# Performance work log

Measured on AMD Instinct MI355X. Metric: run time of the kernel, lower is better.

## Reference

```python
import jax, jax.numpy as jnp
import numpy as np

T, B, V = 512, 64, 1296
S = 30            # fixed target length per sample (targets are concatenated B*S)
BLANK = 0
NEG = -1e30       # -inf surrogate, safe under logaddexp


def setup_inputs() -> dict:
    key = jax.random.key(0)
    k1, k2, k3 = jax.random.split(key, 3)
    logits = jax.random.normal(k1, (T, B, V), dtype=jnp.float32)
    log_probs = jax.nn.log_softmax(logits, axis=-1)  # valid log-prob input to CTC
    # targets are gloss ids in [1, V) (blank=0 excluded), concatenated layout
    targets = jax.random.randint(k2, (B * S,), 1, V, dtype=jnp.int64)
    input_lengths = jax.random.randint(k3, (B,), T // 2, T + 1, dtype=jnp.int32)
    target_lengths = jnp.full((B,), S, dtype=jnp.int32)
    return {"log_probs": log_probs, "targets": targets,
            "input_lengths": input_lengths, "target_lengths": target_lengths}


def _ctc_loss(log_probs, targets2d, input_lengths, target_lengths):
    # log_probs: (T,B,V); targets2d: (B,S)
    L = 2 * S + 1
    b_idx = jnp.arange(B)
    # extended label sequence with interleaved blanks: (B, L)
    ext = jnp.zeros((B, L), dtype=targets2d.dtype).at[:, 1::2].set(targets2d)
    # emission log-probs on lattice positions: lp[t,b,l] = log_probs[t,b,ext[b,l]]
    lp = jnp.take_along_axis(log_probs,
                             jnp.broadcast_to(ext[None, :, :], (T, B, L)), axis=2)
    # skip transition allowed where ext[l] != blank and ext[l] != ext[l-2]
    ext_m2 = jnp.pad(ext[:, :-2], ((0, 0), (2, 0)), constant_values=BLANK)
    allow = (ext != BLANK) & (ext != ext_m2)  # (B, L)

    alpha0 = jnp.full((B, L), NEG, dtype=log_probs.dtype)
    alpha0 = alpha0.at[:, 0].set(lp[0, :, 0]).at[:, 1].set(lp[0, :, 1])

    def step(alpha, lp_t):
        prev1 = jnp.pad(alpha[:, :-1], ((0, 0), (1, 0)), constant_values=NEG)
        prev2 = jnp.pad(alpha[:, :-2], ((0, 0), (2, 0)), constant_values=NEG)
        m = jnp.logaddexp(alpha, prev1)
        m = jnp.where(allow, jnp.logaddexp(m, prev2), m)
        new = m + lp_t
        return new, new

    _, alphas = jax.lax.scan(step, alpha0, lp[1:])          # (T-1, B, L)
    alphas = jnp.concatenate([alpha0[None], alphas], axis=0)  # (T, B, L)

    # alpha at each sample's final frame
    alpha_T = alphas[input_lengths - 1, b_idx]               # (B, L)
    tl = target_lengths.astype(jnp.int32)
    a_last_blank = alpha_T[b_idx, 2 * tl]
    a_last_label = alpha_T[b_idx, 2 * tl - 1]
    loss = -jnp.logaddexp(a_last_blank, a_last_label)        # (B,)
    # zero_infinity=True: infeasible alignments contribute 0
    loss = jnp.where(loss >= 1e29, 0.0, loss)
    # reduction='mean': per-sample loss / target_length, then batch mean
    return jnp.mean(loss / target_lengths.astype(loss.dtype))


def reference(log_probs, targets, input_lengths, target_lengths):
    targets2d = targets.reshape(B, S)  # all target_lengths == S (concatenated layout)
    return _ctc_loss(log_probs, targets2d, input_lengths, target_lengths)
```

## Files before the change

kernel.cpp:

```cpp
#include <hip/hip_runtime.h>

#define T_DIM 512
#define B_DIM 64
#define V_DIM 1296
#define S_DIM 30
#define LN2   0.6931471805599453f

typedef float v2f __attribute__((ext_vector_type(2)));

template<int CTRL, bool BC>
__device__ __forceinline__ float dppf(float src, float old) {
    return __int_as_float(__builtin_amdgcn_update_dpp(
        __float_as_int(old), __float_as_int(src), CTRL, 0xF, 0xF, BC));
}

template<int MODE>
__device__ __forceinline__ void consume_chunk(const float4* __restrict__ ringc,
                                              int c, int len, int lane, v2f S,
                                              v2f& X, v2f& Y, int& E)
{
    const int jl = lane & 15;
    float4 buf[8];
#pragma unroll
    for (int i = 0; i < 8; ++i) buf[i] = ringc[i * 16 + jl];

    float mred = 0.f;
#pragma unroll
    for (int i = 0; i < 32; ++i) {
        float4 w = buf[i & 7];
        if (i + 8 < 32) buf[i & 7] = ringc[(i + 8) * 16 + jl];

        if (MODE == 0 && i == 0) {
            bool l0 = (lane == 0);
            X = (v2f){ l0 ? ldexpf(w.z, 64) : 0.f, 0.f };
            Y = (v2f){ l0 ? ldexpf(w.x, 64) : 0.f, 0.f };
            E = 64;
        } else {
            float q3m = dppf<0x111, true>(Y.y, 0.f);
            v2f Z  = { q3m, Y.x };
            v2f T1 = X + Z;
            v2f T2 = X + Y;
            v2f T3 = __builtin_elementwise_fma(S, Z, T2);
            v2f Wb = { w.z, w.w };
            v2f Wl = { w.x, w.y };
            v2f Xn = T1 * Wb;
            v2f Yn = T3 * Wl;
            if (MODE == 2) {
                bool act = (c * 32 + i) < len;
                X = act ? Xn : X;
                Y = act ? Yn : Y;
            } else { X = Xn; Y = Yn; }
        }

        if ((i & 7) == 3) mred = fmaxf(fmaxf(X.x, X.y), fmaxf(Y.x, Y.y));
        if ((i & 7) == 4) mred = fmaxf(mred, dppf<0x111, true>(mred, 0.f));
        if ((i & 7) == 5) mred = fmaxf(mred, dppf<0x112, true>(mred, 0.f));
        if ((i & 7) == 6) mred = fmaxf(mred, dppf<0x114, true>(mred, 0.f));
        if ((i & 7) == 7) {
            mred = fmaxf(mred, dppf<0x118, true>(mred, 0.f));
            int e15 = (__builtin_amdgcn_readlane(__float_as_int(mred), 15) >> 23) & 0xFF;
            int s = 191 - e15;
            X = (v2f){ ldexpf(X.x, s), ldexpf(X.y, s) };
            Y = (v2f){ ldexpf(Y.x, s), ldexpf(Y.y, s) };
            E += s;
        }
    }
}

struct PReg { float a, b, c; };

__device__ __forceinline__ PReg load_rows(const float* __restrict__ lpb,
                                          int k, int r, int lab0, int lab1)
{
    const float* row = lpb + (size_t)(k * 32 + r) * (B_DIM * V_DIM);
    PReg x;
    x.a = row[lab0];
    x.b = row[lab1];
    x.c = row[0];
    return x;
}

__device__ __forceinline__ void write_chunk(float4* __restrict__ ring, int k, int p,
                                            int q, const PReg& x)
{
    float wz = __expf(x.c);
    float wx = (q < 15) ? __expf(x.a) : 0.f;
    float wy = (q < 15) ? __expf(x.b) : 0.f;
    ring[(size_t)(k & 3) * 512 + p] = make_float4(wx, wy, wz, wz);
}

__global__ __launch_bounds__(576)
void ctc_fused_kernel(const float* __restrict__ log_probs,
                      const int*   __restrict__ targets,
                      const int*   __restrict__ input_lengths,
                      const int*   __restrict__ target_lengths,
                      float*       __restrict__ losses,
                      unsigned*    __restrict__ counter,
                      float*       __restrict__ out)
{
    __shared__ float4 ring[4 * 512];
    const int  b    = blockIdx.x;
    const int  tid  = threadIdx.x;
    const int  len  = input_lengths[b];
    const bool prod = (tid < 512);

    const int q = tid & 15;
    const int r = (tid & 511) >> 4;
    int lab0 = 0, lab1 = 0;
    PReg rA = {0,0,0}, rB = {0,0,0};
    const float* lpb = log_probs + (size_t)b * V_DIM;

    const int lane = tid - 512;
    v2f X = {0.f, 0.f}, Y = {0.f, 0.f}, S = {0.f, 0.f};
    int E = 0;

    if (prod) {
        int i0 = b * S_DIM + ((2 * q     < S_DIM) ? 2 * q     : 0);
        int i1 = b * S_DIM + ((2 * q + 1 < S_DIM) ? 2 * q + 1 : 0);
        lab0 = targets[i0];
        lab1 = targets[i1];
        PReg t0 = load_rows(lpb, 0, r, lab0, lab1);
        PReg t1 = load_rows(lpb, 1, r, lab0, lab1);
        PReg t2 = load_rows(lpb, 2, r, lab0, lab1);
        rA = load_rows(lpb, 3, r, lab0, lab1);
        rB = load_rows(lpb, 4, r, lab0, lab1);
        write_chunk(ring, 0, tid, q, t0);
        write_chunk(ring, 1, tid, q, t1);
        write_chunk(ring, 2, tid, q, t2);
        asm volatile("s_waitcnt lgkmcnt(0)" ::: "memory");
    } else {
        int lq = lane & 15;
        float s0 = 0.f, s1 = 0.f;
        if (lq < 15) {
            int k0 = 2 * lq;
            int tc = targets[b * S_DIM + k0];
            int tp = (k0 > 0) ? targets[b * S_DIM + k0 - 1] : -1;
            s0 = (tc != tp) ? 1.f : 0.f;
            int tn = targets[b * S_DIM + k0 + 1];
            s1 = (tn != tc) ? 1.f : 0.f;
        }
        S = (v2f){ s0, s1 };
    }
    __builtin_amdgcn_s_barrier();
    __builtin_amdgcn_sched_barrier(0);

    for (int c = 0; c < 16; ++c) {
        if (prod) {
            if (c < 13) write_chunk(ring, c + 3, tid, q, rA);
            PReg nl = {0,0,0};
            if (c < 11) nl = load_rows(lpb, c + 5, r, lab0, lab1);
            rA = rB; rB = nl;
            asm volatile("s_waitcnt lgkmcnt(0)" ::: "memory");
        } else {
            const float4* ringc = &ring[(size_t)(c & 3) * 512];
            if (c == 0)                   consume_chunk<0>(ringc, c, len, lane, S, X, Y, E);
            else if ((c + 1) * 32 <= len) consume_chunk<1>(ringc, c, len, lane, S, X, Y, E);
            else if (c * 32 < len)        consume_chunk<2>(ringc, c, len, lane, S, X, Y, E);
        }
        __builtin_amdgcn_s_barrier();
        __builtin_amdgcn_sched_barrier(0);
    }

    if (!prod) {
        int tl   = target_lengths[b];
        int pB_p = 2 * tl, pL_p = 2 * tl - 1;
        float vB = (pB_p & 2) ? ((pB_p & 1) ? Y.y : X.y) : ((pB_p & 1) ? Y.x : X.x);
        float vL = (pL_p & 2) ? ((pL_p & 1) ? Y.y : X.y) : ((pL_p & 1) ? Y.x : X.x);
        float pB = __shfl(vB, pB_p >> 2);
        float pL = __shfl(vL, pL_p >> 2);
        float loss = -LN2 * (__builtin_amdgcn_logf(pB + pL) - (float)E);
        if (!(loss < 1e29f)) loss = 0.f;
        loss /= (float)tl;

        unsigned old = 0;
        if (lane == 0) {
            losses[b] = loss;
            __threadfence();
            old = atomicAdd(counter, 1u);
        }
        old = __shfl(old, 0);
        if (old == 63u) {
            __threadfence();
            float v = ((volatile const float*)losses)[lane];
#pragma unroll
            for (int off = 32; off >= 1; off >>= 1)
                v += __shfl_xor(v, off);
            if (lane == 0) out[0] = v * (1.f / (float)B_DIM);
        }
    }
}

extern "C" void kernel_launch(void* const* d_in, const int* in_sizes, int n_in,
                              void* d_out, int out_size, void* d_ws, size_t ws_size,
                              hipStream_t stream)
{
    const float* log_probs      = (const float*)d_in[0];
    const int*   targets        = (const int*)  d_in[1];
    const int*   input_lengths  = (const int*)  d_in[2];
    const int*   target_lengths = (const int*)  d_in[3];
    float*       out            = (float*)d_out;
    float*       losses         = (float*)d_ws;
    unsigned*    counter        = (unsigned*)((char*)d_ws + 256);

    hipMemsetAsync(counter, 0, sizeof(unsigned), stream);
    hipLaunchKernelGGL(ctc_fused_kernel, dim3(B_DIM), dim3(576), 0, stream,
                       log_probs, targets, input_lengths, target_lengths,
                       losses, counter, out);
}
```

Baseline: 35.16 us.

## Split CTC into parallel gather/exp kernel and scan kernel over compact buffer

```diff
diff --git a/kernel.cpp b/kernel.cpp
--- a/kernel.cpp
+++ b/kernel.cpp
@@ -67,36 +67,64 @@
     }
 }
 
-struct PReg { float a, b, c; };
-
-__device__ __forceinline__ PReg load_rows(const float* __restrict__ lpb,
-                                          int k, int r, int lab0, int lab1)
-{
-    const float* row = lpb + (size_t)(k * 32 + r) * (B_DIM * V_DIM);
-    PReg x;
-    x.a = row[lab0];
-    x.b = row[lab1];
-    x.c = row[0];
-    return x;
-}
-
-__device__ __forceinline__ void write_chunk(float4* __restrict__ ring, int k, int p,
-                                            int q, const PReg& x)
-{
-    float wz = __expf(x.c);
-    float wx = (q < 15) ? __expf(x.a) : 0.f;
-    float wy = (q < 15) ? __expf(x.b) : 0.f;
-    ring[(size_t)(k & 3) * 512 + p] = make_float4(wx, wy, wz, wz);
+__global__ __launch_bounds__(512)
+void ctc_gather_kernel(const float* __restrict__ log_probs,
+                       const int*   __restrict__ targets,
+                       const int*   __restrict__ input_lengths,
+                       float4*      __restrict__ compact,
+                       unsigned*    __restrict__ counter)
+{
+    const int bid = blockIdx.x;
+    const int b   = bid >> 2;
+    const int qt  = bid & 3;
+    const int tid = threadIdx.x;
+    const int s   = tid & 15;
+    const int ri  = tid >> 4;
+    const int len = input_lengths[b];
+    if (bid == 0 && tid == 0) *counter = 0u;
+
+    int lab0 = 0, lab1 = 0;
+    if (s < 15) {
+        lab0 = targets[b * S_DIM + 2 * s];
+        lab1 = targets[b * S_DIM + 2 * s + 1];
+    }
+    const float* lpb = log_probs + (size_t)b * V_DIM;
+
+    float va[4], vb[4], vc[4];
+    int   trow[4];
+    bool  act[4];
+#pragma unroll
+    for (int k = 0; k < 4; ++k) {
+        int t = qt * 128 + k * 32 + ri;
+        trow[k] = t;
+        act[k]  = (t < len);
+        if (act[k]) {
+            const float* row = lpb + (size_t)t * (B_DIM * V_DIM);
+            va[k] = row[lab0];
+            vb[k] = row[lab1];
+            vc[k] = row[0];
+        }
+    }
+#pragma unroll
+    for (int k = 0; k < 4; ++k) {
+        if (act[k]) {
+            float wb = __expf(vc[k]);
+            float w0 = (s < 15) ? __expf(va[k]) : 0.f;
+            float w1 = (s < 15) ? __expf(vb[k]) : 0.f;
+            compact[((size_t)b * T_DIM + trow[k]) * 16 + s] =
+                make_float4(w0, w1, wb, wb);
+        }
+    }
 }
 
 __global__ __launch_bounds__(576)
-void ctc_fused_kernel(const float* __restrict__ log_probs,
-                      const int*   __restrict__ targets,
-                      const int*   __restrict__ input_lengths,
-                      const int*   __restrict__ target_lengths,
-                      float*       __restrict__ losses,
-                      unsigned*    __restrict__ counter,
-                      float*       __restrict__ out)
+void ctc_scan_kernel(const float4* __restrict__ compact,
+                     const int*    __restrict__ targets,
+                     const int*    __restrict__ input_lengths,
+                     const int*    __restrict__ target_lengths,
+                     float*        __restrict__ losses,
+                     unsigned*     __restrict__ counter,
+                     float*        __restrict__ out)
 {
     __shared__ float4 ring[4 * 512];
     const int  b    = blockIdx.x;
@@ -104,29 +132,22 @@
     const int  len  = input_lengths[b];
     const bool prod = (tid < 512);
 
-    const int q = tid & 15;
-    const int r = (tid & 511) >> 4;
-    int lab0 = 0, lab1 = 0;
-    PReg rA = {0,0,0}, rB = {0,0,0};
-    const float* lpb = log_probs + (size_t)b * V_DIM;
-
+    const float4* cb = compact + (size_t)b * T_DIM * 16;
+
+    float4 fA = {0,0,0,0}, fB = {0,0,0,0};
     const int lane = tid - 512;
     v2f X = {0.f, 0.f}, Y = {0.f, 0.f}, S = {0.f, 0.f};
     int E = 0;
 
     if (prod) {
-        int i0 = b * S_DIM + ((2 * q     < S_DIM) ? 2 * q     : 0);
-        int i1 = b * S_DIM + ((2 * q + 1 < S_DIM) ? 2 * q + 1 : 0);
-        lab0 = targets[i0];
-        lab1 = targets[i1];
-        PReg t0 = load_rows(lpb, 0, r, lab0, lab1);
-        PReg t1 = load_rows(lpb, 1, r, lab0, lab1);
-        PReg t2 = load_rows(lpb, 2, r, lab0, lab1);
-        rA = load_rows(lpb, 3, r, lab0, lab1);
-        rB = load_rows(lpb, 4, r, lab0, lab1);
-        write_chunk(ring, 0, tid, q, t0);
-        write_chunk(ring, 1, tid, q, t1);
-        write_chunk(ring, 2, tid, q, t2);
+        float4 t0 = cb[0 * 512 + tid];
+        float4 t1 = cb[1 * 512 + tid];
+        float4 t2 = cb[2 * 512 + tid];
+        fA = cb[3 * 512 + tid];
+        fB = cb[4 * 512 + tid];
+        ring[0 * 512 + tid] = t0;
+        ring[1 * 512 + tid] = t1;
+        ring[2 * 512 + tid] = t2;
         asm volatile("s_waitcnt lgkmcnt(0)" ::: "memory");
     } else {
         int lq = lane & 15;
@@ -146,13 +167,13 @@
 
     for (int c = 0; c < 16; ++c) {
         if (prod) {
-            if (c < 13) write_chunk(ring, c + 3, tid, q, rA);
-            PReg nl = {0,0,0};
-            if (c < 11) nl = load_rows(lpb, c + 5, r, lab0, lab1);
-            rA = rB; rB = nl;
+            if (c < 13) ring[((c + 3) & 3) * 512 + tid] = fA;
+            float4 nl = {0,0,0,0};
+            if (c < 11) nl = cb[(size_t)(c + 5) * 512 + tid];
+            fA = fB; fB = nl;
             asm volatile("s_waitcnt lgkmcnt(0)" ::: "memory");
         } else {
-            const float4* ringc = &ring[(size_t)(c & 3) * 512];
+            const float4* ringc = &ring[(c & 3) * 512];
             if (c == 0)                   consume_chunk<0>(ringc, c, len, lane, S, X, Y, E);
             else if ((c + 1) * 32 <= len) consume_chunk<1>(ringc, c, len, lane, S, X, Y, E);
             else if (c * 32 < len)        consume_chunk<2>(ringc, c, len, lane, S, X, Y, E);
@@ -199,11 +220,14 @@
     const int*   input_lengths  = (const int*)  d_in[2];
     const int*   target_lengths = (const int*)  d_in[3];
     float*       out            = (float*)d_out;
-    float*       losses         = (float*)d_ws;
-    unsigned*    counter        = (unsigned*)((char*)d_ws + 256);
-
-    hipMemsetAsync(counter, 0, sizeof(unsigned), stream);
-    hipLaunchKernelGGL(ctc_fused_kernel, dim3(B_DIM), dim3(576), 0, stream,
-                       log_probs, targets, input_lengths, target_lengths,
+
+    float4*   compact = (float4*)d_ws;
+    float*    losses  = (float*)((char*)d_ws + (size_t)8 * 1024 * 1024);
+    unsigned* counter = (unsigned*)((char*)d_ws + (size_t)8 * 1024 * 1024 + 256);
+
+    hipLaunchKernelGGL(ctc_gather_kernel, dim3(256), dim3(512), 0, stream,
+                       log_probs, targets, input_lengths, compact, counter);
+    hipLaunchKernelGGL(ctc_scan_kernel, dim3(B_DIM), dim3(576), 0, stream,
+                       compact, targets, input_lengths, target_lengths,
                        losses, counter, out);
 }
```

After: 36.09 us. 1.03x slower.

## Replace lockstep barrier pipeline with per-chunk flag handoff between producer and consumer waves

Applied to the files above, without the earlier changes.

```diff
diff --git a/kernel.cpp b/kernel.cpp
--- a/kernel.cpp
+++ b/kernel.cpp
@@ -15,25 +15,28 @@
 }
 
 template<int MODE>
-__device__ __forceinline__ void consume_chunk(const float4* __restrict__ ringc,
+__device__ __forceinline__ void consume_chunk(const float2* __restrict__ wl,
+                                              const float*  __restrict__ wb,
                                               int c, int len, int lane, v2f S,
                                               v2f& X, v2f& Y, int& E)
 {
     const int jl = lane & 15;
-    float4 buf[8];
-#pragma unroll
-    for (int i = 0; i < 8; ++i) buf[i] = ringc[i * 16 + jl];
+    float2 bl[8];
+    float  bb[8];
+#pragma unroll
+    for (int i = 0; i < 8; ++i) { bl[i] = wl[i * 16 + jl]; bb[i] = wb[i]; }
 
     float mred = 0.f;
 #pragma unroll
     for (int i = 0; i < 32; ++i) {
-        float4 w = buf[i & 7];
-        if (i + 8 < 32) buf[i & 7] = ringc[(i + 8) * 16 + jl];
+        float2 wv  = bl[i & 7];
+        float  wbv = bb[i & 7];
+        if (i + 8 < 32) { bl[i & 7] = wl[(i + 8) * 16 + jl]; bb[i & 7] = wb[i + 8]; }
 
         if (MODE == 0 && i == 0) {
             bool l0 = (lane == 0);
-            X = (v2f){ l0 ? ldexpf(w.z, 64) : 0.f, 0.f };
-            Y = (v2f){ l0 ? ldexpf(w.x, 64) : 0.f, 0.f };
+            X = (v2f){ l0 ? ldexpf(wbv, 64) : 0.f, 0.f };
+            Y = (v2f){ l0 ? ldexpf(wv.x, 64) : 0.f, 0.f };
             E = 64;
         } else {
             float q3m = dppf<0x111, true>(Y.y, 0.f);
@@ -41,8 +44,8 @@
             v2f T1 = X + Z;
             v2f T2 = X + Y;
             v2f T3 = __builtin_elementwise_fma(S, Z, T2);
-            v2f Wb = { w.z, w.w };
-            v2f Wl = { w.x, w.y };
+            v2f Wb = { wbv, wbv };
+            v2f Wl = { wv.x, wv.y };
             v2f Xn = T1 * Wb;
             v2f Yn = T3 * Wl;
             if (MODE == 2) {
@@ -59,34 +62,12 @@
         if ((i & 7) == 7) {
             mred = fmaxf(mred, dppf<0x118, true>(mred, 0.f));
             int e15 = (__builtin_amdgcn_readlane(__float_as_int(mred), 15) >> 23) & 0xFF;
-            int s = 191 - e15;
-            X = (v2f){ ldexpf(X.x, s), ldexpf(X.y, s) };
-            Y = (v2f){ ldexpf(Y.x, s), ldexpf(Y.y, s) };
-            E += s;
+            int sfx = 191 - e15;
+            X = (v2f){ ldexpf(X.x, sfx), ldexpf(X.y, sfx) };
+            Y = (v2f){ ldexpf(Y.x, sfx), ldexpf(Y.y, sfx) };
+            E += sfx;
         }
     }
-}
-
-struct PReg { float a, b, c; };
-
-__device__ __forceinline__ PReg load_rows(const float* __restrict__ lpb,
-                                          int k, int r, int lab0, int lab1)
-{
-    const float* row = lpb + (size_t)(k * 32 + r) * (B_DIM * V_DIM);
-    PReg x;
-    x.a = row[lab0];
-    x.b = row[lab1];
-    x.c = row[0];
-    return x;
-}
-
-__device__ __forceinline__ void write_chunk(float4* __restrict__ ring, int k, int p,
-                                            int q, const PReg& x)
-{
-    float wz = __expf(x.c);
-    float wx = (q < 15) ? __expf(x.a) : 0.f;
-    float wy = (q < 15) ? __expf(x.b) : 0.f;
-    ring[(size_t)(k & 3) * 512 + p] = make_float4(wx, wy, wz, wz);
 }
 
 __global__ __launch_bounds__(576)
@@ -98,76 +79,113 @@
                       unsigned*    __restrict__ counter,
                       float*       __restrict__ out)
 {
-    __shared__ float4 ring[4 * 512];
-    const int  b    = blockIdx.x;
-    const int  tid  = threadIdx.x;
-    const int  len  = input_lengths[b];
-    const bool prod = (tid < 512);
-
-    const int q = tid & 15;
-    const int r = (tid & 511) >> 4;
-    int lab0 = 0, lab1 = 0;
-    PReg rA = {0,0,0}, rB = {0,0,0};
-    const float* lpb = log_probs + (size_t)b * V_DIM;
-
-    const int lane = tid - 512;
-    v2f X = {0.f, 0.f}, Y = {0.f, 0.f}, S = {0.f, 0.f};
-    int E = 0;
-
-    if (prod) {
-        int i0 = b * S_DIM + ((2 * q     < S_DIM) ? 2 * q     : 0);
-        int i1 = b * S_DIM + ((2 * q + 1 < S_DIM) ? 2 * q + 1 : 0);
-        lab0 = targets[i0];
-        lab1 = targets[i1];
-        PReg t0 = load_rows(lpb, 0, r, lab0, lab1);
-        PReg t1 = load_rows(lpb, 1, r, lab0, lab1);
-        PReg t2 = load_rows(lpb, 2, r, lab0, lab1);
-        rA = load_rows(lpb, 3, r, lab0, lab1);
-        rB = load_rows(lpb, 4, r, lab0, lab1);
-        write_chunk(ring, 0, tid, q, t0);
-        write_chunk(ring, 1, tid, q, t1);
-        write_chunk(ring, 2, tid, q, t2);
-        asm volatile("s_waitcnt lgkmcnt(0)" ::: "memory");
+    __shared__ float2   ring_wl[8 * 32 * 16];
+    __shared__ float    ring_wb[8 * 32];
+    __shared__ unsigned flags[16];
+    __shared__ unsigned consumed;
+
+    const int b    = blockIdx.x;
+    const int tid  = threadIdx.x;
+    const int len  = input_lengths[b];
+    const int w    = tid >> 6;
+    const int lane = tid & 63;
+
+    if (tid < 16) flags[tid] = 0u;
+    if (tid == 16) consumed = 0u;
+    __syncthreads();
+
+    if (w < 8) {
+        const int s  = lane & 15;
+        const int r0 = lane >> 4;
+        int labA = 0, labB = 0;
+        if (s < 15) {
+            labA = targets[b * S_DIM + 2 * s];
+            labB = targets[b * S_DIM + 2 * s + 1];
+        }
+        const float* lpb = log_probs + (size_t)b * V_DIM;
+
+        float vA[2][8], vB[2][8];
+#pragma unroll
+        for (int h = 0; h < 2; ++h) {
+            const int c = w + 8 * h;
+#pragma unroll
+            for (int k = 0; k < 8; ++k) {
+                int r = r0 + 4 * k;
+                int t = c * 32 + r;
+                if (t < len) {
+                    const float* row = lpb + (size_t)t * (B_DIM * V_DIM);
+                    if (s < 15) { vA[h][k] = row[labA]; vB[h][k] = row[labB]; }
+                    else        { vA[h][k] = row[0];    vB[h][k] = -1e30f;   }
+                } else { vA[h][k] = -1e30f; vB[h][k] = -1e30f; }
+            }
+        }
+#pragma unroll
+        for (int h = 0; h < 2; ++h) {
+            const int c = w + 8 * h;
+            if (h == 1) {
+                unsigned guard = 0;
+                while (__hip_atomic_load(&consumed, __ATOMIC_ACQUIRE,
+                                         __HIP_MEMORY_SCOPE_WORKGROUP) < (unsigned)(w + 1)) {
+                    __builtin_amdgcn_s_sleep(1);
+                    if (++guard > (1u << 18)) break;
+                }
+            }
+            const int slot = c & 7;
+#pragma unroll
+            for (int k = 0; k < 8; ++k) {
+                int r = r0 + 4 * k;
+                if (s < 15) {
+                    ring_wl[slot * 512 + r * 16 + s] =
+                        make_float2(__expf(vA[h][k]), __expf(vB[h][k]));
+                } else {
+                    ring_wb[slot * 32 + r] = __expf(vA[h][k]);
+                    ring_wl[slot * 512 + r * 16 + 15] = make_float2(0.f, 0.f);
+                }
+            }
+            asm volatile("s_waitcnt lgkmcnt(0)" ::: "memory");
+            if (lane == 0)
+                __hip_atomic_store(&flags[c], 1u, __ATOMIC_RELEASE,
+                                   __HIP_MEMORY_SCOPE_WORKGROUP);
+        }
     } else {
-        int lq = lane & 15;
+        const int jl = lane & 15;
+        const int tl = target_lengths[b];
+
         float s0 = 0.f, s1 = 0.f;
-        if (lq < 15) {
-            int k0 = 2 * lq;
+        if (jl < 15) {
+            int k0 = 2 * jl;
             int tc = targets[b * S_DIM + k0];
             int tp = (k0 > 0) ? targets[b * S_DIM + k0 - 1] : -1;
             s0 = (tc != tp) ? 1.f : 0.f;
             int tn = targets[b * S_DIM + k0 + 1];
             s1 = (tn != tc) ? 1.f : 0.f;
         }
-        S = (v2f){ s0, s1 };
-    }
-    __builtin_amdgcn_s_barrier();
-    __builtin_amdgcn_sched_barrier(0);
-
-    for (int c = 0; c < 16; ++c) {
-        if (prod) {
-            if (c < 13) write_chunk(ring, c + 3, tid, q, rA);
-            PReg nl = {0,0,0};
-            if (c < 11) nl = load_rows(lpb, c + 5, r, lab0, lab1);
-            rA = rB; rB = nl;
-            asm volatile("s_waitcnt lgkmcnt(0)" ::: "memory");
-        } else {
-            const float4* ringc = &ring[(size_t)(c & 3) * 512];
-            if (c == 0)                   consume_chunk<0>(ringc, c, len, lane, S, X, Y, E);
-            else if ((c + 1) * 32 <= len) consume_chunk<1>(ringc, c, len, lane, S, X, Y, E);
-            else if (c * 32 < len)        consume_chunk<2>(ringc, c, len, lane, S, X, Y, E);
-        }
-        __builtin_amdgcn_s_barrier();
-        __builtin_amdgcn_sched_barrier(0);
-    }
-
-    if (!prod) {
-        int tl   = target_lengths[b];
+        v2f S = { s0, s1 };
+        v2f X = { 0.f, 0.f }, Y = { 0.f, 0.f };
+        int E = 0;
+
+        for (int c = 0; c < 16; ++c) {
+            if (c * 32 >= len) break;
+            unsigned guard = 0;
+            while (__hip_atomic_load(&flags[c], __ATOMIC_ACQUIRE,
+                                     __HIP_MEMORY_SCOPE_WORKGROUP) == 0u) {
+                __builtin_amdgcn_s_sleep(1);
+                if (++guard > (1u << 18)) break;
+            }
+            const float2* wl = &ring_wl[(c & 7) * 512];
+            const float*  wb = &ring_wb[(c & 7) * 32];
+            if (c == 0)                   consume_chunk<0>(wl, wb, c, len, lane, S, X, Y, E);
+            else if ((c + 1) * 32 <= len) consume_chunk<1>(wl, wb, c, len, lane, S, X, Y, E);
+            else                          consume_chunk<2>(wl, wb, c, len, lane, S, X, Y, E);
+            __hip_atomic_store(&consumed, (unsigned)(c + 1), __ATOMIC_RELEASE,
+                               __HIP_MEMORY_SCOPE_WORKGROUP);
+        }
+
         int pB_p = 2 * tl, pL_p = 2 * tl - 1;
-        float vB = (pB_p & 2) ? ((pB_p & 1) ? Y.y : X.y) : ((pB_p & 1) ? Y.x : X.x);
-        float vL = (pL_p & 2) ? ((pL_p & 1) ? Y.y : X.y) : ((pL_p & 1) ? Y.x : X.x);
-        float pB = __shfl(vB, pB_p >> 2);
-        float pL = __shfl(vL, pL_p >> 2);
+        float vBv = (pB_p & 2) ? ((pB_p & 1) ? Y.y : X.y) : ((pB_p & 1) ? Y.x : X.x);
+        float vLv = (pL_p & 2) ? ((pL_p & 1) ? Y.y : X.y) : ((pL_p & 1) ? Y.x : X.x);
+        float pB = __shfl(vBv, pB_p >> 2);
+        float pL = __shfl(vLv, pL_p >> 2);
         float loss = -LN2 * (__builtin_amdgcn_logf(pB + pL) - (float)E);
         if (!(loss < 1e29f)) loss = 0.f;
         loss /= (float)tl;
```

Measured after the change: 45.75 us. 30.1% more time.
